# Performance work log

Hardware: AMD Instinct MI355X
Metric: run time of the kernel (lower is better)

The kernel has to match this reference:

```python
import jax, jax.numpy as jnp
import numpy as np

N = 256
FEAT = 1024           # box_head.fc7.out_features
HID_REL = 256         # RelationProposalNetwork hidden_dim
GCN_HID = 256         # gcn_hidden
HEADS = 4
NUM_PARTS = 20
OUT = NUM_PARTS + 1
TOPK = 3
IN_GCN = FEAT + 4


def setup_inputs() -> dict:
    key = jax.random.key(0)
    ks = jax.random.split(key, 16)
    features = jax.random.normal(ks[0], (N, FEAT), jnp.float32)
    # valid pixel-space boxes (x1, y1, x2, y2) inside an 800x800 image
    xy = jax.random.uniform(ks[1], (N, 2), jnp.float32, 0.0, 700.0)
    wh = jax.random.uniform(ks[2], (N, 2), jnp.float32, 8.0, 100.0)
    boxes = jnp.concatenate([xy, xy + wh], axis=1)
    s = 0.02
    W_fc1 = jax.random.normal(ks[3], (2 * FEAT + 4, HID_REL), jnp.float32) * s
    b_fc1 = jnp.zeros((HID_REL,), jnp.float32)
    W_fc2 = jax.random.normal(ks[4], (HID_REL, 1), jnp.float32) * s
    b_fc2 = jnp.zeros((1,), jnp.float32)
    W1 = jax.random.normal(ks[5], (IN_GCN, HEADS * GCN_HID), jnp.float32) * s
    a_src1 = jax.random.normal(ks[6], (HEADS, GCN_HID), jnp.float32) * s
    a_dst1 = jax.random.normal(ks[7], (HEADS, GCN_HID), jnp.float32) * s
    b1 = jnp.zeros((HEADS * GCN_HID,), jnp.float32)
    W2 = jax.random.normal(ks[8], (HEADS * GCN_HID, OUT), jnp.float32) * s
    a_src2 = jax.random.normal(ks[9], (1, OUT), jnp.float32) * s
    a_dst2 = jax.random.normal(ks[10], (1, OUT), jnp.float32) * s
    b2 = jnp.zeros((OUT,), jnp.float32)
    return {
        "features": features, "boxes": boxes,
        "W_fc1": W_fc1, "b_fc1": b_fc1, "W_fc2": W_fc2, "b_fc2": b_fc2,
        "W1": W1, "a_src1": a_src1, "a_dst1": a_dst1, "b1": b1,
        "W2": W2, "a_src2": a_src2, "a_dst2": a_dst2, "b2": b2,
        "img_h": 800, "img_w": 800,
    }


def _gat_layer(x, W, a_src, a_dst, bias, s, t, n, heads, ch):
    # PyG GATConv: message flows edge_index[0] (s) -> edge_index[1] (t),
    # softmax over incoming edges of each target node t.
    h = (x @ W).reshape(n, heads, ch)                       # [n, H, C]
    e = jax.nn.leaky_relu(
        jnp.einsum("ehc,hc->eh", h[s], a_src)
        + jnp.einsum("ehc,hc->eh", h[t], a_dst), 0.2)        # [E, H]
    m = jnp.full((n, heads), -1e30, e.dtype).at[t].max(e)    # segment max
    p = jnp.exp(e - m[t])
    denom = jax.ops.segment_sum(p, t, num_segments=n)
    alpha = p / denom[t]                                     # [E, H]
    out = jax.ops.segment_sum(alpha[:, :, None] * h[s], t, num_segments=n)
    return out.reshape(n, heads * ch) + bias


def _forward(features, boxes, W_fc1, b_fc1, W_fc2, b_fc2,
             W1, a_src1, a_dst1, b1, W2, a_src2, a_dst2, b2, img_h, img_w):
    n = features.shape[0]
    # --- RelationProposalNetwork: dense O(N^2) pairwise MLP ---
    f1 = jnp.broadcast_to(features[:, None, :], (n, n, FEAT))
    f2 = jnp.broadcast_to(features[None, :, :], (n, n, FEAT))
    geom = jnp.abs(boxes[:, None, :] - boxes[None, :, :])    # [n, n, 4]
    pair = jnp.concatenate([f1, f2, geom], axis=-1)          # [n, n, 2052]
    hid = jax.nn.relu(pair @ W_fc1 + b_fc1)                  # [n, n, 256]
    rel = (hid @ W_fc2 + b_fc2)[..., 0]                      # [n, n]
    # --- top-k graph construction (drop first = self, as in source) ---
    idx = jax.lax.top_k(rel, TOPK + 1)[1][:, 1:]             # [n, topk]
    s_e = jnp.repeat(jnp.arange(n), TOPK)                    # edge_index[0]
    t_e = idx.reshape(-1)                                    # edge_index[1]
    loops = jnp.arange(n)                                    # GATConv add_self_loops
    s_e = jnp.concatenate([s_e, loops])
    t_e = jnp.concatenate([t_e, loops])
    # --- normalized box geometry node features ---
    scale = jnp.array([img_w, img_h, img_w, img_h], jnp.float32)
    nb = boxes / scale
    geomn = jnp.stack([nb[:, 0], nb[:, 1], nb[:, 2] - nb[:, 0], nb[:, 3] - nb[:, 1]], axis=1)
    gcn_in = jnp.concatenate([features, geomn], axis=1)      # [n, 1028]
    # --- AttentionalGCN: GAT(heads=4) -> ReLU -> GAT(heads=1) ---
    h1 = jax.nn.relu(_gat_layer(gcn_in, W1, a_src1, a_dst1, b1, s_e, t_e, n, HEADS, GCN_HID))
    logits = _gat_layer(h1, W2, a_src2, a_dst2, b2, s_e, t_e, n, 1, OUT)
    return logits


def reference(features, boxes, W_fc1, b_fc1, W_fc2, b_fc2,
              W1, a_src1, a_dst1, b1, W2, a_src2, a_dst2, b2, img_h, img_w):
    logits = _forward(features, boxes, W_fc1, b_fc1, W_fc2, b_fc2,
                      W1, a_src1, a_dst1, b1, W2, a_src2, a_dst2, b2, img_h, img_w)
    labels = jnp.argmax(logits, axis=1)
    return logits, labels
```

## Files before the change

kernel.cpp:

```cpp
#include <hip/hip_runtime.h>
#include <math.h>

#define NN 256
#define FEAT 1024
#define HIDR 256
#define HEADS 4
#define GCNH 256
#define M1 1024
#define OUTC 21
#define MAXDEG (NN + 1)
#define KC 8
#define KCH (FEAT / KC)
#define FCOLS 1536

__global__ __launch_bounds__(256) void k_big(
        const float* __restrict__ feat, const float* __restrict__ Wfc1,
        const float* __restrict__ W1, float* __restrict__ P) {
    __shared__ float fS[8][KCH];
    int rg = blockIdx.x, cg = blockIdx.y, kc = blockIdx.z;
    int tid = threadIdx.x;
    int r0 = rg * 8, k0 = kc * KCH;
    for (int x = tid; x < 8 * KCH; x += 256) {
        int r = x >> 7, kk = x & (KCH - 1);
        fS[r][kk] = feat[(size_t)(r0 + r) * FEAT + k0 + kk];
    }
    __syncthreads();
    int gc = cg * 512 + tid * 2;
    const float* pW;
    int ld;
    if (gc < 256)      { pW = Wfc1 + (size_t)k0 * HIDR + gc;                  ld = HIDR; }
    else if (gc < 512) { pW = Wfc1 + (size_t)(FEAT + k0) * HIDR + (gc - 256); ld = HIDR; }
    else               { pW = W1   + (size_t)k0 * M1 + (gc - 512);            ld = M1;   }
    float2 acc[8];
#pragma unroll
    for (int r = 0; r < 8; r++) { acc[r].x = 0.f; acc[r].y = 0.f; }
    float2 w0 = *(const float2*)(pW);
    float2 w1 = *(const float2*)(pW + ld);
    float2 w2 = *(const float2*)(pW + 2 * ld);
    float2 w3 = *(const float2*)(pW + 3 * ld);
    for (int kk = 0; kk < KCH; kk += 4) {
        pW += 4 * ld;
        float2 n0 = *(const float2*)(pW);
        float2 n1 = *(const float2*)(pW + ld);
        float2 n2 = *(const float2*)(pW + 2 * ld);
        float2 n3 = *(const float2*)(pW + 3 * ld);
#pragma unroll
        for (int r = 0; r < 8; r++) {
            float4 f = *(const float4*)&fS[r][kk];
            acc[r].x = fmaf(f.x, w0.x, acc[r].x); acc[r].y = fmaf(f.x, w0.y, acc[r].y);
            acc[r].x = fmaf(f.y, w1.x, acc[r].x); acc[r].y = fmaf(f.y, w1.y, acc[r].y);
            acc[r].x = fmaf(f.z, w2.x, acc[r].x); acc[r].y = fmaf(f.z, w2.y, acc[r].y);
            acc[r].x = fmaf(f.w, w3.x, acc[r].x); acc[r].y = fmaf(f.w, w3.y, acc[r].y);
        }
        w0 = n0; w1 = n1; w2 = n2; w3 = n3;
    }
    float* Pp = P + ((size_t)kc * NN + r0) * FCOLS + gc;
#pragma unroll
    for (int r = 0; r < 8; r++)
        *(float2*)(Pp + (size_t)r * FCOLS) = acc[r];
}

__global__ __launch_bounds__(384) void k_redfix(
        const float* __restrict__ P, const float* __restrict__ bfc1,
        const float* __restrict__ boxes, const int* __restrict__ imh,
        const int* __restrict__ imw, const float* __restrict__ W1,
        const float* __restrict__ as1, const float* __restrict__ ad1,
        float* __restrict__ A, float* __restrict__ BT4,
        float* __restrict__ hpre, float* __restrict__ es1,
        float* __restrict__ ed1, float* __restrict__ geomn) {
    __shared__ float gS[4];
    int row = blockIdx.x, tid = threadIdx.x;
    int c4 = tid * 4;
    const float* p = P + (size_t)row * FCOLS + c4;
    const size_t str = (size_t)NN * FCOLS;
    float4 t0 = *(const float4*)(p);
    float4 t1 = *(const float4*)(p + str);
    float4 t2 = *(const float4*)(p + 2 * str);
    float4 t3 = *(const float4*)(p + 3 * str);
    float4 t4 = *(const float4*)(p + 4 * str);
    float4 t5 = *(const float4*)(p + 5 * str);
    float4 t6 = *(const float4*)(p + 6 * str);
    float4 t7 = *(const float4*)(p + 7 * str);
    float4 s;
    s.x = ((t0.x + t1.x) + (t2.x + t3.x)) + ((t4.x + t5.x) + (t6.x + t7.x));
    s.y = ((t0.y + t1.y) + (t2.y + t3.y)) + ((t4.y + t5.y) + (t6.y + t7.y));
    s.z = ((t0.z + t1.z) + (t2.z + t3.z)) + ((t4.z + t5.z) + (t6.z + t7.z));
    s.w = ((t0.w + t1.w) + (t2.w + t3.w)) + ((t4.w + t5.w) + (t6.w + t7.w));
    if (tid == 0) {
        float w = (float)imw[0], h = (float)imh[0];
        float x1 = boxes[row * 4 + 0] / w, y1 = boxes[row * 4 + 1] / h;
        float x2 = boxes[row * 4 + 2] / w, y2 = boxes[row * 4 + 3] / h;
        gS[0] = x1; gS[1] = y1; gS[2] = x2 - x1; gS[3] = y2 - y1;
        geomn[row * 4 + 0] = x1;
        geomn[row * 4 + 1] = y1;
        geomn[row * 4 + 2] = x2 - x1;
        geomn[row * 4 + 3] = y2 - y1;
    }
    __syncthreads();
    if (c4 < 256) {
        float4 b = *(const float4*)(bfc1 + c4);
        s.x += b.x; s.y += b.y; s.z += b.z; s.w += b.w;
        *(float4*)(A + (size_t)row * HIDR + c4) = s;
    } else if (c4 < 512) {
        int kk = c4 - 256;
        *(float4*)(BT4 + (size_t)(kk >> 2) * (NN * 4) + row * 4) = s;
    } else {
        int ch = c4 - 512;
        float g0 = gS[0], g1 = gS[1], g2 = gS[2], g3 = gS[3];
        float4 wv;
        wv = *(const float4*)(W1 + (size_t)(FEAT + 0) * M1 + ch);
        s.x = fmaf(g0, wv.x, s.x); s.y = fmaf(g0, wv.y, s.y);
        s.z = fmaf(g0, wv.z, s.z); s.w = fmaf(g0, wv.w, s.w);
        wv = *(const float4*)(W1 + (size_t)(FEAT + 1) * M1 + ch);
        s.x = fmaf(g1, wv.x, s.x); s.y = fmaf(g1, wv.y, s.y);
        s.z = fmaf(g1, wv.z, s.z); s.w = fmaf(g1, wv.w, s.w);
        wv = *(const float4*)(W1 + (size_t)(FEAT + 2) * M1 + ch);
        s.x = fmaf(g2, wv.x, s.x); s.y = fmaf(g2, wv.y, s.y);
        s.z = fmaf(g2, wv.z, s.z); s.w = fmaf(g2, wv.w, s.w);
        wv = *(const float4*)(W1 + (size_t)(FEAT + 3) * M1 + ch);
        s.x = fmaf(g3, wv.x, s.x); s.y = fmaf(g3, wv.y, s.y);
        s.z = fmaf(g3, wv.z, s.z); s.w = fmaf(g3, wv.w, s.w);
        *(float4*)(hpre + (size_t)row * M1 + ch) = s;
        float4 a = *(const float4*)(as1 + ch);
        float4 b = *(const float4*)(ad1 + ch);
        float ps = s.x * a.x + s.y * a.y + s.z * a.z + s.w * a.w;
        float pd = s.x * b.x + s.y * b.y + s.z * b.z + s.w * b.w;
#pragma unroll
        for (int o = 32; o > 0; o >>= 1) {
            ps += __shfl_down(ps, o);
            pd += __shfl_down(pd, o);
        }
        if ((tid & 63) == 0) {
            int head = (tid - 128) >> 6;
            es1[row * 4 + head] = ps;
            ed1[row * 4 + head] = pd;
        }
    }
}

__global__ __launch_bounds__(512) void k_reltopk(
        const float* __restrict__ A, const float* __restrict__ BT4,
        const float* __restrict__ boxes, const float* __restrict__ Wfc1,
        const float* __restrict__ Wfc2, int* __restrict__ idxTop) {
    __shared__ float As[HIDR], w2s[HIDR], wg0[HIDR], wg1[HIDR], wg2[HIDR], wg3[HIDR];
    __shared__ float sval[512];
    __shared__ unsigned long long swk[8];
    __shared__ int win;
    int i = blockIdx.x, tid = threadIdx.x;
    int j = tid & 255, half = tid >> 8;
    if (tid < 256) {
        As[tid]  = A[i * HIDR + tid];
        w2s[tid] = Wfc2[tid];
        wg0[tid] = Wfc1[(size_t)(2 * FEAT + 0) * HIDR + tid];
    } else {
        int q = tid - 256;
        wg1[q] = Wfc1[(size_t)(2 * FEAT + 1) * HIDR + q];
        wg2[q] = Wfc1[(size_t)(2 * FEAT + 2) * HIDR + q];
        wg3[q] = Wfc1[(size_t)(2 * FEAT + 3) * HIDR + q];
    }
    float bi0 = boxes[i * 4 + 0], bi1 = boxes[i * 4 + 1];
    float bi2 = boxes[i * 4 + 2], bi3 = boxes[i * 4 + 3];
    float g0 = fabsf(bi0 - boxes[j * 4 + 0]);
    float g1 = fabsf(bi1 - boxes[j * 4 + 1]);
    float g2 = fabsf(bi2 - boxes[j * 4 + 2]);
    float g3 = fabsf(bi3 - boxes[j * 4 + 3]);
    __syncthreads();
    int k0 = half * 128;
    const float* pB = BT4 + (size_t)(k0 >> 2) * (NN * 4) + j * 4;
    float acc = 0.f;
    for (int kk = k0; kk < k0 + 128; kk += 4) {
        float4 a4 = *(const float4*)&As[kk];
        float4 w4 = *(const float4*)&w2s[kk];
        float4 q0 = *(const float4*)&wg0[kk];
        float4 q1 = *(const float4*)&wg1[kk];
        float4 q2 = *(const float4*)&wg2[kk];
        float4 q3 = *(const float4*)&wg3[kk];
        float4 b4 = *(const float4*)pB;
        pB += NN * 4;
        float v;
        v = a4.x + b4.x; v = fmaf(g0, q0.x, v); v = fmaf(g1, q1.x, v);
        v = fmaf(g2, q2.x, v); v = fmaf(g3, q3.x, v);
        acc = fmaf(fmaxf(v, 0.f), w4.x, acc);
        v = a4.y + b4.y; v = fmaf(g0, q0.y, v); v = fmaf(g1, q1.y, v);
        v = fmaf(g2, q2.y, v); v = fmaf(g3, q3.y, v);
        acc = fmaf(fmaxf(v, 0.f), w4.y, acc);
        v = a4.z + b4.z; v = fmaf(g0, q0.z, v); v = fmaf(g1, q1.z, v);
        v = fmaf(g2, q2.z, v); v = fmaf(g3, q3.z, v);
        acc = fmaf(fmaxf(v, 0.f), w4.z, acc);
        v = a4.w + b4.w; v = fmaf(g0, q0.w, v); v = fmaf(g1, q1.w, v);
        v = fmaf(g2, q2.w, v); v = fmaf(g3, q3.w, v);
        acc = fmaf(fmaxf(v, 0.f), w4.w, acc);
    }
    sval[tid] = acc;
    __syncthreads();
    if (tid < 256) sval[tid] = sval[tid] + sval[tid + 256];
    __syncthreads();
    for (int r = 0; r < 4; r++) {
        unsigned long long key = 0ULL;
        if (tid < 256) {
            unsigned u = __float_as_uint(sval[tid]);
            u = (u & 0x80000000u) ? ~u : (u | 0x80000000u);
            key = ((unsigned long long)u << 32) | (unsigned)(NN - 1 - tid);
        }
#pragma unroll
        for (int o = 32; o > 0; o >>= 1) {
            unsigned long long nk = __shfl_down(key, o);
            if (nk > key) key = nk;
        }
        if ((tid & 63) == 0) swk[tid >> 6] = key;
        __syncthreads();
        if (tid == 0) {
            unsigned long long m = swk[0];
#pragma unroll
            for (int q = 1; q < 8; q++) if (swk[q] > m) m = swk[q];
            int wj = NN - 1 - (int)(m & 0xFFFFFFFFu);
            win = wj;
            if (r > 0) idxTop[i * 3 + (r - 1)] = wj;
        }
        __syncthreads();
        if (tid == win) sval[tid] = -1e38f;
        __syncthreads();
    }
}

__global__ __launch_bounds__(256) void k_gat1h2(
        const float* __restrict__ idxTopF, const float* __restrict__ hpre,
        const float* __restrict__ es1, const float* __restrict__ ed1,
        const float* __restrict__ b1, const float* __restrict__ W2,
        const float* __restrict__ as2, const float* __restrict__ ad2,
        int* __restrict__ deg, int* __restrict__ inlist,
        float* __restrict__ h2, float* __restrict__ es2,
        float* __restrict__ ed2) {
    const int* idxTop = (const int*)idxTopF;
    __shared__ int pfx[NN];
    __shared__ int lst[MAXDEG];
    __shared__ int dgS;
    __shared__ float sc[MAXDEG * 4];
    __shared__ float mh[4], dh[4];
    __shared__ float sh[M1];
    __shared__ float part[12 * OUTC];
    __shared__ float h2row[OUTC];
    int t = blockIdx.x, tid = threadIdx.x;
    int f = (idxTop[tid * 3 + 0] == t) | (idxTop[tid * 3 + 1] == t)
          | (idxTop[tid * 3 + 2] == t);
    pfx[tid] = f;
    __syncthreads();
    for (int o = 1; o < NN; o <<= 1) {
        int add = (tid >= o) ? pfx[tid - o] : 0;
        __syncthreads();
        pfx[tid] += add;
        __syncthreads();
    }
    if (f) {
        lst[pfx[tid] - 1] = tid;
        inlist[t * MAXDEG + (pfx[tid] - 1)] = tid;
    }
    if (tid == NN - 1) {
        int d = pfx[NN - 1];
        lst[d] = t;
        inlist[t * MAXDEG + d] = t;
        dgS = d + 1;
        deg[t] = d + 1;
    }
    __syncthreads();
    int dg = dgS;
    for (int p = tid; p < dg * 4; p += 256) {
        int e = p >> 2, h = p & 3;
        int s = lst[e];
        float v = es1[s * 4 + h] + ed1[t * 4 + h];
        sc[p] = v >= 0.f ? v : 0.2f * v;
    }
    __syncthreads();
    if (tid < 4) {
        float m = -1e30f;
        for (int e = 0; e < dg; e++) m = fmaxf(m, sc[e * 4 + tid]);
        float s = 0.f;
        for (int e = 0; e < dg; e++) s += expf(sc[e * 4 + tid] - m);
        mh[tid] = m; dh[tid] = s;
    }
    __syncthreads();
    for (int p = tid; p < dg * 4; p += 256) {
        int h = p & 3;
        sc[p] = expf(sc[p] - mh[h]) / dh[h];
    }
    __syncthreads();
    float acc[4] = {0.f, 0.f, 0.f, 0.f};
    for (int e = 0; e < dg; e++) {
        int s = lst[e];
        const float* hs = hpre + (size_t)s * M1;
#pragma unroll
        for (int q = 0; q < 4; q++)
            acc[q] = fmaf(sc[e * 4 + q], hs[q * GCNH + tid], acc[q]);
    }
#pragma unroll
    for (int q = 0; q < 4; q++) {
        int c = q * GCNH + tid;
        sh[c] = fmaxf(acc[q] + b1[c], 0.f);
    }
    __syncthreads();
    if (tid < 252) {
        int o = tid % OUTC, p = tid / OUTC;
        float a2 = 0.f;
        for (int d = p; d < M1; d += 12)
            a2 = fmaf(sh[d], W2[d * OUTC + o], a2);
        part[p * OUTC + o] = a2;
    }
    __syncthreads();
    if (tid < OUTC) {
        float s = 0.f;
        for (int p = 0; p < 12; p++) s += part[p * OUTC + tid];
        h2[t * OUTC + tid] = s;
        h2row[tid] = s;
    }
    __syncthreads();
    if (tid == 0) {
        float s = 0.f, dd = 0.f;
        for (int k = 0; k < OUTC; k++) {
            s = fmaf(h2row[k], as2[k], s);
            dd = fmaf(h2row[k], ad2[k], dd);
        }
        es2[t] = s; ed2[t] = dd;
    }
}

__global__ __launch_bounds__(64) void k_gat2(
        const float* __restrict__ h2, const float* __restrict__ es2,
        const float* __restrict__ ed2, const int* __restrict__ deg,
        const int* __restrict__ inlist, const float* __restrict__ b2,
        float* __restrict__ out) {
    __shared__ float sc[MAXDEG];
    __shared__ float md[2];
    __shared__ float lv[OUTC];
    int t = blockIdx.x, tid = threadIdx.x;
    int dg = deg[t];
    float edt = ed2[t];
    for (int p = tid; p < dg; p += 64) {
        int s = inlist[t * MAXDEG + p];
        float v = es2[s] + edt;
        sc[p] = v >= 0.f ? v : 0.2f * v;
    }
    __syncthreads();
    if (tid == 0) {
        float m = -1e30f;
        for (int e = 0; e < dg; e++) m = fmaxf(m, sc[e]);
        float s = 0.f;
        for (int e = 0; e < dg; e++) s += expf(sc[e] - m);
        md[0] = m; md[1] = s;
    }
    __syncthreads();
    if (tid < OUTC) {
        float acc = 0.f;
        for (int e = 0; e < dg; e++) {
            int s = inlist[t * MAXDEG + e];
            float a = expf(sc[e] - md[0]) / md[1];
            acc = fmaf(a, h2[s * OUTC + tid], acc);
        }
        float v = acc + b2[tid];
        out[t * OUTC + tid] = v;
        lv[tid] = v;
    }
    __syncthreads();
    if (tid == 0) {
        int best = 0;
        float bv = lv[0];
        for (int o = 1; o < OUTC; o++)
            if (lv[o] > bv) { bv = lv[o]; best = o; }
        out[NN * OUTC + t] = (float)best;
    }
}

extern "C" void kernel_launch(void* const* d_in, const int* in_sizes, int n_in,
                              void* d_out, int out_size, void* d_ws,
                              size_t ws_size, hipStream_t stream) {
    const float* feat  = (const float*)d_in[0];
    const float* boxes = (const float*)d_in[1];
    const float* Wfc1  = (const float*)d_in[2];
    const float* bfc1  = (const float*)d_in[3];
    const float* Wfc2  = (const float*)d_in[4];
    const float* bfc2  = (const float*)d_in[5];   (void)bfc2;
    const float* W1    = (const float*)d_in[6];
    const float* as1   = (const float*)d_in[7];
    const float* ad1   = (const float*)d_in[8];
    const float* b1    = (const float*)d_in[9];
    const float* W2    = (const float*)d_in[10];
    const float* as2   = (const float*)d_in[11];
    const float* ad2   = (const float*)d_in[12];
    const float* b2    = (const float*)d_in[13];
    const int*   imh   = (const int*)d_in[14];
    const int*   imw   = (const int*)d_in[15];

    float* ws = (float*)d_ws;
    float* P     = ws;  ws += KC * NN * FCOLS;
    float* A     = ws;  ws += NN * HIDR;
    float* BT4   = ws;  ws += NN * HIDR;
    float* hpre  = ws;  ws += NN * M1;
    float* es1   = ws;  ws += NN * 4;
    float* ed1   = ws;  ws += NN * 4;
    float* h2    = ws;  ws += NN * OUTC;
    float* es2   = ws;  ws += NN;
    float* ed2   = ws;  ws += NN;
    float* geomn = ws;  ws += NN * 4;
    int* deg     = (int*)ws;
    int* inlist  = deg + NN;
    int* idxTop  = inlist + NN * MAXDEG;

    float* out = (float*)d_out;

    k_big<<<dim3(32, 3, KC), 256, 0, stream>>>(feat, Wfc1, W1, P);
    k_redfix<<<NN, 384, 0, stream>>>(P, bfc1, boxes, imh, imw, W1, as1, ad1,
                                     A, BT4, hpre, es1, ed1, geomn);
    k_reltopk<<<NN, 512, 0, stream>>>(A, BT4, boxes, Wfc1, Wfc2, idxTop);
    k_gat1h2<<<NN, 256, 0, stream>>>((const float*)idxTop, hpre, es1, ed1,
                                     b1, W2, as2, ad2, deg, inlist,
                                     h2, es2, ed2);
    k_gat2<<<NN, 64, 0, stream>>>(h2, es2, ed2, deg, inlist, b2, out);
}
```

Measured before the change: 163.2 us.

## Enlarge GEMM row tile, drop geomn writes, use ballot-based compaction in GAT

```diff
diff --git a/kernel.cpp b/kernel.cpp
--- a/kernel.cpp
+++ b/kernel.cpp
@@ -11,29 +11,30 @@
 #define MAXDEG (NN + 1)
 #define KC 8
 #define KCH (FEAT / KC)
+#define RB 16
 #define FCOLS 1536
 
 __global__ __launch_bounds__(256) void k_big(
         const float* __restrict__ feat, const float* __restrict__ Wfc1,
         const float* __restrict__ W1, float* __restrict__ P) {
-    __shared__ float fS[8][KCH];
-    int rg = blockIdx.x, cg = blockIdx.y, kc = blockIdx.z;
+    __shared__ float fS[RB][KCH];
+    int rg = blockIdx.x, cgy = blockIdx.y, kc = blockIdx.z;
     int tid = threadIdx.x;
-    int r0 = rg * 8, k0 = kc * KCH;
-    for (int x = tid; x < 8 * KCH; x += 256) {
+    int r0 = rg * RB, k0 = kc * KCH;
+    for (int x = tid; x < RB * KCH; x += 256) {
         int r = x >> 7, kk = x & (KCH - 1);
         fS[r][kk] = feat[(size_t)(r0 + r) * FEAT + k0 + kk];
     }
     __syncthreads();
-    int gc = cg * 512 + tid * 2;
+    int gc = cgy * 512 + tid * 2;
     const float* pW;
     int ld;
     if (gc < 256)      { pW = Wfc1 + (size_t)k0 * HIDR + gc;                  ld = HIDR; }
     else if (gc < 512) { pW = Wfc1 + (size_t)(FEAT + k0) * HIDR + (gc - 256); ld = HIDR; }
     else               { pW = W1   + (size_t)k0 * M1 + (gc - 512);            ld = M1;   }
-    float2 acc[8];
-#pragma unroll
-    for (int r = 0; r < 8; r++) { acc[r].x = 0.f; acc[r].y = 0.f; }
+    float2 acc[RB];
+#pragma unroll
+    for (int r = 0; r < RB; r++) { acc[r].x = 0.f; acc[r].y = 0.f; }
     float2 w0 = *(const float2*)(pW);
     float2 w1 = *(const float2*)(pW + ld);
     float2 w2 = *(const float2*)(pW + 2 * ld);
@@ -45,7 +46,7 @@
         float2 n2 = *(const float2*)(pW + 2 * ld);
         float2 n3 = *(const float2*)(pW + 3 * ld);
 #pragma unroll
-        for (int r = 0; r < 8; r++) {
+        for (int r = 0; r < RB; r++) {
             float4 f = *(const float4*)&fS[r][kk];
             acc[r].x = fmaf(f.x, w0.x, acc[r].x); acc[r].y = fmaf(f.x, w0.y, acc[r].y);
             acc[r].x = fmaf(f.y, w1.x, acc[r].x); acc[r].y = fmaf(f.y, w1.y, acc[r].y);
@@ -56,7 +57,7 @@
     }
     float* Pp = P + ((size_t)kc * NN + r0) * FCOLS + gc;
 #pragma unroll
-    for (int r = 0; r < 8; r++)
+    for (int r = 0; r < RB; r++)
         *(float2*)(Pp + (size_t)r * FCOLS) = acc[r];
 }
 
@@ -67,8 +68,7 @@
         const float* __restrict__ as1, const float* __restrict__ ad1,
         float* __restrict__ A, float* __restrict__ BT4,
         float* __restrict__ hpre, float* __restrict__ es1,
-        float* __restrict__ ed1, float* __restrict__ geomn) {
-    __shared__ float gS[4];
+        float* __restrict__ ed1) {
     int row = blockIdx.x, tid = threadIdx.x;
     int c4 = tid * 4;
     const float* p = P + (size_t)row * FCOLS + c4;
@@ -86,17 +86,6 @@
     s.y = ((t0.y + t1.y) + (t2.y + t3.y)) + ((t4.y + t5.y) + (t6.y + t7.y));
     s.z = ((t0.z + t1.z) + (t2.z + t3.z)) + ((t4.z + t5.z) + (t6.z + t7.z));
     s.w = ((t0.w + t1.w) + (t2.w + t3.w)) + ((t4.w + t5.w) + (t6.w + t7.w));
-    if (tid == 0) {
-        float w = (float)imw[0], h = (float)imh[0];
-        float x1 = boxes[row * 4 + 0] / w, y1 = boxes[row * 4 + 1] / h;
-        float x2 = boxes[row * 4 + 2] / w, y2 = boxes[row * 4 + 3] / h;
-        gS[0] = x1; gS[1] = y1; gS[2] = x2 - x1; gS[3] = y2 - y1;
-        geomn[row * 4 + 0] = x1;
-        geomn[row * 4 + 1] = y1;
-        geomn[row * 4 + 2] = x2 - x1;
-        geomn[row * 4 + 3] = y2 - y1;
-    }
-    __syncthreads();
     if (c4 < 256) {
         float4 b = *(const float4*)(bfc1 + c4);
         s.x += b.x; s.y += b.y; s.z += b.z; s.w += b.w;
@@ -105,8 +94,11 @@
         int kk = c4 - 256;
         *(float4*)(BT4 + (size_t)(kk >> 2) * (NN * 4) + row * 4) = s;
     } else {
+        float w = (float)imw[0], h = (float)imh[0];
+        float x1 = boxes[row * 4 + 0] / w, y1 = boxes[row * 4 + 1] / h;
+        float x2 = boxes[row * 4 + 2] / w, y2 = boxes[row * 4 + 3] / h;
+        float g0 = x1, g1 = y1, g2 = x2 - x1, g3 = y2 - y1;
         int ch = c4 - 512;
-        float g0 = gS[0], g1 = gS[1], g2 = gS[2], g3 = gS[3];
         float4 wv;
         wv = *(const float4*)(W1 + (size_t)(FEAT + 0) * M1 + ch);
         s.x = fmaf(g0, wv.x, s.x); s.y = fmaf(g0, wv.y, s.y);
@@ -232,38 +224,35 @@
         float* __restrict__ h2, float* __restrict__ es2,
         float* __restrict__ ed2) {
     const int* idxTop = (const int*)idxTopF;
-    __shared__ int pfx[NN];
+    __shared__ int wcnt[4];
     __shared__ int lst[MAXDEG];
-    __shared__ int dgS;
     __shared__ float sc[MAXDEG * 4];
     __shared__ float mh[4], dh[4];
     __shared__ float sh[M1];
     __shared__ float part[12 * OUTC];
     __shared__ float h2row[OUTC];
     int t = blockIdx.x, tid = threadIdx.x;
+    int wv = tid >> 6, ln = tid & 63;
     int f = (idxTop[tid * 3 + 0] == t) | (idxTop[tid * 3 + 1] == t)
           | (idxTop[tid * 3 + 2] == t);
-    pfx[tid] = f;
-    __syncthreads();
-    for (int o = 1; o < NN; o <<= 1) {
-        int add = (tid >= o) ? pfx[tid - o] : 0;
-        __syncthreads();
-        pfx[tid] += add;
-        __syncthreads();
-    }
+    unsigned long long m = __ballot(f != 0);
+    if (ln == 0) wcnt[wv] = __popcll(m);
+    __syncthreads();
+    int c0 = wcnt[0], c1 = wcnt[1], c2 = wcnt[2], c3 = wcnt[3];
+    int woff = (wv > 0 ? c0 : 0) + (wv > 1 ? c1 : 0) + (wv > 2 ? c2 : 0);
+    int dg = c0 + c1 + c2 + c3;
     if (f) {
-        lst[pfx[tid] - 1] = tid;
-        inlist[t * MAXDEG + (pfx[tid] - 1)] = tid;
-    }
-    if (tid == NN - 1) {
-        int d = pfx[NN - 1];
-        lst[d] = t;
-        inlist[t * MAXDEG + d] = t;
-        dgS = d + 1;
-        deg[t] = d + 1;
-    }
-    __syncthreads();
-    int dg = dgS;
+        int slot = woff + __popcll(m & ((1ULL << ln) - 1ULL));
+        lst[slot] = tid;
+        inlist[t * MAXDEG + slot] = tid;
+    }
+    if (tid == 0) {
+        lst[dg] = t;
+        inlist[t * MAXDEG + dg] = t;
+        deg[t] = dg + 1;
+    }
+    dg += 1;
+    __syncthreads();
     for (int p = tid; p < dg * 4; p += 256) {
         int e = p >> 2, h = p & 3;
         int s = lst[e];
@@ -272,11 +261,11 @@
     }
     __syncthreads();
     if (tid < 4) {
-        float m = -1e30f;
-        for (int e = 0; e < dg; e++) m = fmaxf(m, sc[e * 4 + tid]);
+        float mm = -1e30f;
+        for (int e = 0; e < dg; e++) mm = fmaxf(mm, sc[e * 4 + tid]);
         float s = 0.f;
-        for (int e = 0; e < dg; e++) s += expf(sc[e * 4 + tid] - m);
-        mh[tid] = m; dh[tid] = s;
+        for (int e = 0; e < dg; e++) s += expf(sc[e * 4 + tid] - mm);
+        mh[tid] = mm; dh[tid] = s;
     }
     __syncthreads();
     for (int p = tid; p < dg * 4; p += 256) {
@@ -399,16 +388,15 @@
     float* h2    = ws;  ws += NN * OUTC;
     float* es2   = ws;  ws += NN;
     float* ed2   = ws;  ws += NN;
-    float* geomn = ws;  ws += NN * 4;
     int* deg     = (int*)ws;
     int* inlist  = deg + NN;
     int* idxTop  = inlist + NN * MAXDEG;
 
     float* out = (float*)d_out;
 
-    k_big<<<dim3(32, 3, KC), 256, 0, stream>>>(feat, Wfc1, W1, P);
+    k_big<<<dim3(NN / RB, 3, KC), 256, 0, stream>>>(feat, Wfc1, W1, P);
     k_redfix<<<NN, 384, 0, stream>>>(P, bfc1, boxes, imh, imw, W1, as1, ad1,
-                                     A, BT4, hpre, es1, ed1, geomn);
+                                     A, BT4, hpre, es1, ed1);
     k_reltopk<<<NN, 512, 0, stream>>>(A, BT4, boxes, Wfc1, Wfc2, idxTop);
     k_gat1h2<<<NN, 256, 0, stream>>>((const float*)idxTop, hpre, es1, ed1,
                                      b1, W2, as2, ad2, deg, inlist,
```

After: 167.5 us. 2.7% more time.
